# Optimization experiments

Hardware: AMD Instinct MI355X
Metric: run time of the kernel (lower is better)

## Reference

```python
import jax, jax.numpy as jnp
import numpy as np

EMB_DIM = 1024
N_HEADS = 16
HEAD_DIM = EMB_DIM // N_HEADS
WINDOW = 128
B, T = 4, 2048


def setup_inputs() -> dict:
    key = jax.random.key(0)
    k1, k2, k3 = jax.random.split(key, 3)
    x = jax.random.normal(k1, (B, T, EMB_DIM), dtype=jnp.float32)
    # nn.Linear weights: stored as [out, in], applied as x @ W^T
    s1 = 1.0 / np.sqrt(EMB_DIM)
    w_qkv = jax.random.uniform(k2, (3 * EMB_DIM, EMB_DIM), jnp.float32, -s1, s1)
    w_out = jax.random.uniform(k3, (EMB_DIM, EMB_DIM), jnp.float32, -s1, s1)
    return {"x": x, "w_qkv": w_qkv, "w_out": w_out}


def reference(x, w_qkv, w_out):
    Bs, Ts, C = x.shape
    scale = HEAD_DIM ** -0.5
    qkv = x @ w_qkv.T                                   # [B,T,3C]
    qkv = qkv.reshape(Bs, Ts, 3, N_HEADS, HEAD_DIM)
    qkv = jnp.transpose(qkv, (2, 0, 3, 1, 4))           # [3,B,H,T,D]
    q, k, v = qkv[0], qkv[1], qkv[2]
    scores = jnp.einsum('bhtd,bhsd->bhts', q, k) * scale  # [B,H,T,T]
    i = jnp.arange(Ts)[:, None]
    j = jnp.arange(Ts)[None, :]
    # causal AND within sliding window: i - WINDOW <= j <= i
    allowed = (j <= i) & (j >= i - WINDOW)               # [T,T] bool
    scores = jnp.where(allowed[None, None], scores, -jnp.inf)
    attn = jax.nn.softmax(scores, axis=-1)
    out = jnp.einsum('bhts,bhsd->bhtd', attn, v)         # [B,H,T,D]
    out = jnp.transpose(out, (0, 2, 1, 3)).reshape(Bs, Ts, C)
    return out @ w_out.T
```

## Files before the change

### kernel.cpp

```cpp
#include <hip/hip_runtime.h>
#include <hip/hip_bf16.h>
#include <stdint.h>

typedef __attribute__((ext_vector_type(8))) short bf16x8;
typedef __attribute__((ext_vector_type(4))) float f32x4;
typedef __attribute__((ext_vector_type(4))) unsigned short u16x4;

#define B_ 4
#define T_ 2048
#define C_ 1024
#define H_ 16
#define D_ 64

__device__ __forceinline__ unsigned short f2bf(float f) {
  union { float f; uint32_t u; } v; v.f = f;
  uint32_t u = v.u;
  uint32_t r = (u + 0x7FFFu + ((u >> 16) & 1u)) >> 16;
  return (unsigned short)r;
}

__device__ __forceinline__ void gload_lds16(const unsigned short* g, short* l) {
  __builtin_amdgcn_global_load_lds((__attribute__((address_space(1))) void*)(uintptr_t)g,
                                   (__attribute__((address_space(3))) void*)l, 16, 0, 0);
}

__global__ void __launch_bounds__(256) cast_f32_bf16(const float* __restrict__ src,
                                                     unsigned short* __restrict__ dst,
                                                     int n4) {
  int i = blockIdx.x * 256 + threadIdx.x;
  if (i >= n4) return;
  float4 f = ((const float4*)src)[i];
  u16x4 o;
  o[0] = f2bf(f.x); o[1] = f2bf(f.y); o[2] = f2bf(f.z); o[3] = f2bf(f.w);
  ((u16x4*)dst)[i] = o;
}

template <int MODE>
__global__ void __launch_bounds__(256) gemm_bt(const unsigned short* __restrict__ A,
                                               const unsigned short* __restrict__ Bm,
                                               unsigned short* __restrict__ qb,
                                               unsigned short* __restrict__ kb,
                                               unsigned short* __restrict__ vb,
                                               float* __restrict__ fo) {
  __shared__ short As[128 * 32];
  __shared__ short Bs[128 * 32];
  const int tid = threadIdx.x;
  const int bm = blockIdx.y * 128;
  const int bn = blockIdx.x * 128;
  const int w = tid >> 6;
  const int l = tid & 63;
  const int wm = w >> 1, wn = w & 1;
  const int lm = l & 15, lq = l >> 4;

  const int srow = w * 16 + (l >> 2);
  const int scol = (l & 3) * 8;
  const unsigned short* gA0 = A + (size_t)(bm + srow) * 1024 + scol;
  const unsigned short* gA1 = gA0 + (size_t)64 * 1024;
  const unsigned short* gB0 = Bm + (size_t)(bn + srow) * 1024 + scol;
  const unsigned short* gB1 = gB0 + (size_t)64 * 1024;
  short* dA0 = As + w * 512;
  short* dA1 = As + 2048 + w * 512;
  short* dB0 = Bs + w * 512;
  short* dB1 = Bs + 2048 + w * 512;

  f32x4 acc[4][4];
#pragma unroll
  for (int i = 0; i < 4; i++)
#pragma unroll
    for (int j = 0; j < 4; j++) acc[i][j] = (f32x4){0.f, 0.f, 0.f, 0.f};

  for (int k0 = 0; k0 < 1024; k0 += 32) {
    __syncthreads();
    gload_lds16(gA0 + k0, dA0);
    gload_lds16(gA1 + k0, dA1);
    gload_lds16(gB0 + k0, dB0);
    gload_lds16(gB1 + k0, dB1);
    __syncthreads();
    bf16x8 af[4], bfr[4];
#pragma unroll
    for (int i = 0; i < 4; i++)
      af[i] = *(const bf16x8*)&As[(wm * 64 + 16 * i + lm) * 32 + 8 * lq];
#pragma unroll
    for (int j = 0; j < 4; j++)
      bfr[j] = *(const bf16x8*)&Bs[(wn * 64 + 16 * j + lm) * 32 + 8 * lq];
#pragma unroll
    for (int i = 0; i < 4; i++)
#pragma unroll
      for (int j = 0; j < 4; j++)
        acc[i][j] = __builtin_amdgcn_mfma_f32_16x16x32_bf16(af[i], bfr[j], acc[i][j], 0, 0, 0);
  }

#pragma unroll
  for (int i = 0; i < 4; i++) {
#pragma unroll
    for (int j = 0; j < 4; j++) {
#pragma unroll
      for (int r = 0; r < 4; r++) {
        int m = bm + wm * 64 + 16 * i + 4 * lq + r;
        int n = bn + wn * 64 + 16 * j + lm;
        float val = acc[i][j][r];
        if (MODE == 0) {
          int which = n >> 10, rem = n & 1023;
          int h = rem >> 6, d = rem & 63;
          int b = m >> 11, t = m & 2047;
          unsigned short* dst = (which == 0) ? qb : ((which == 1) ? kb : vb);
          dst[(((size_t)(b * 16 + h)) * 2048 + t) * 64 + d] = f2bf(val);
        } else {
          fo[(size_t)m * 1024 + n] = val;
        }
      }
    }
  }
}

__global__ void __launch_bounds__(256) transpose_v(const unsigned short* __restrict__ Vb,
                                                   unsigned short* __restrict__ Vt) {
  __shared__ unsigned short Ls[64 * 66];
  const int tid = threadIdx.x;
  const int bh = blockIdx.y;
  const int t0 = blockIdx.x * 64;
  const size_t base = (size_t)bh * (T_ * D_);
  const int d0 = (tid & 7) * 8;
  const int it = tid >> 3;
#pragma unroll
  for (int p = 0; p < 2; p++) {
    int t = it + 32 * p;
    bf16x8 v = *(const bf16x8*)(Vb + base + (size_t)(t0 + t) * 64 + d0);
#pragma unroll
    for (int e = 0; e < 8; e++) Ls[(d0 + e) * 66 + t] = (unsigned short)v[e];
  }
  __syncthreads();
  const int d = tid >> 2;
  const int c = tid & 3;
  uint32_t r[8];
  const uint32_t* Lw = (const uint32_t*)&Ls[d * 66 + c * 16];
#pragma unroll
  for (int wj = 0; wj < 8; wj++) r[wj] = Lw[wj];
  unsigned short* o = Vt + base + (size_t)d * T_ + t0 + c * 16;
  *(uint4*)o = *(const uint4*)&r[0];
  *(uint4*)(o + 8) = *(const uint4*)&r[4];
}

__global__ void __launch_bounds__(256) attn_swa(const unsigned short* __restrict__ Qb,
                                               const unsigned short* __restrict__ Kb,
                                               const unsigned short* __restrict__ Vt,
                                               unsigned short* __restrict__ Ob) {
  __shared__ short P[4][16 * 40];
  const int wv = threadIdx.x >> 6;
  const int l = threadIdx.x & 63;
  const int wid = blockIdx.x * 4 + wv;
  const int bh = wid >> 7;
  const int t0 = (wid & 127) << 4;
  const int lm = l & 15, lq = l >> 4;
  const size_t base = (size_t)bh * (T_ * D_);

  bf16x8 aq0 = *(const bf16x8*)(Qb + base + (size_t)(t0 + lm) * 64 + 8 * lq);
  bf16x8 aq1 = *(const bf16x8*)(Qb + base + (size_t)(t0 + lm) * 64 + 32 + 8 * lq);

  float mst[4], lst[4];
  f32x4 Oa[4];
#pragma unroll
  for (int r = 0; r < 4; r++) { mst[r] = -1e30f; lst[r] = 0.f; }
#pragma unroll
  for (int jt = 0; jt < 4; jt++) Oa[jt] = (f32x4){0.f, 0.f, 0.f, 0.f};

  const float cs = 0.125f * 1.44269504f;
  int jstart = t0 - 128; if (jstart < 0) jstart = 0;

  for (int j0 = jstart; j0 < t0 + 16; j0 += 32) {
    f32x4 S[2];
#pragma unroll
    for (int hh = 0; hh < 2; hh++) {
      int kr = j0 + 16 * hh + lm; if (kr > T_ - 1) kr = T_ - 1;
      bf16x8 bk0 = *(const bf16x8*)(Kb + base + (size_t)kr * 64 + 8 * lq);
      bf16x8 bk1 = *(const bf16x8*)(Kb + base + (size_t)kr * 64 + 32 + 8 * lq);
      f32x4 s = (f32x4){0.f, 0.f, 0.f, 0.f};
      s = __builtin_amdgcn_mfma_f32_16x16x32_bf16(aq0, bk0, s, 0, 0, 0);
      s = __builtin_amdgcn_mfma_f32_16x16x32_bf16(aq1, bk1, s, 0, 0, 0);
      S[hh] = s;
    }
    float p0s[4], p1s[4], al[4];
#pragma unroll
    for (int r = 0; r < 4; r++) {
      int t = t0 + 4 * lq + r;
      int ja = j0 + lm, jb = j0 + 16 + lm;
      float s0 = ((ja <= t) && (ja + 128 >= t)) ? S[0][r] * cs : -1e30f;
      float s1 = ((jb <= t) && (jb + 128 >= t)) ? S[1][r] * cs : -1e30f;
      float m2 = fmaxf(s0, s1);
#pragma unroll
      for (int off = 1; off < 16; off <<= 1) m2 = fmaxf(m2, __shfl_xor(m2, off));
      float mn = fmaxf(mst[r], m2);
      float a = __builtin_amdgcn_exp2f(mst[r] - mn);
      float p0 = __builtin_amdgcn_exp2f(s0 - mn);
      float p1 = __builtin_amdgcn_exp2f(s1 - mn);
      float ps = p0 + p1;
#pragma unroll
      for (int off = 1; off < 16; off <<= 1) ps += __shfl_xor(ps, off);
      lst[r] = lst[r] * a + ps;
      mst[r] = mn;
      al[r] = a; p0s[r] = p0; p1s[r] = p1;
    }
#pragma unroll
    for (int jt = 0; jt < 4; jt++)
#pragma unroll
      for (int r = 0; r < 4; r++) Oa[jt][r] *= al[r];
#pragma unroll
    for (int r = 0; r < 4; r++) {
      P[wv][(4 * lq + r) * 40 + lm] = (short)f2bf(p0s[r]);
      P[wv][(4 * lq + r) * 40 + 16 + lm] = (short)f2bf(p1s[r]);
    }
    bf16x8 pa = *(const bf16x8*)&P[wv][lm * 40 + 8 * lq];
    int tb = j0 + 8 * lq;
    if (tb > T_ - 8) tb = T_ - 8;
#pragma unroll
    for (int jt = 0; jt < 4; jt++) {
      bf16x8 vf = *(const bf16x8*)(Vt + base + (size_t)(16 * jt + lm) * T_ + tb);
      Oa[jt] = __builtin_amdgcn_mfma_f32_16x16x32_bf16(pa, vf, Oa[jt], 0, 0, 0);
    }
  }
  const int b = bh >> 4, h = bh & 15;
#pragma unroll
  for (int r = 0; r < 4; r++) {
    float inv = 1.0f / lst[r];
    int t = t0 + 4 * lq + r;
#pragma unroll
    for (int jt = 0; jt < 4; jt++) {
      int c = h * 64 + 16 * jt + lm;
      Ob[((size_t)(b * T_ + t)) * 1024 + c] = f2bf(Oa[jt][r] * inv);
    }
  }
}

extern "C" void kernel_launch(void* const* d_in, const int* in_sizes, int n_in,
                              void* d_out, int out_size, void* d_ws, size_t ws_size,
                              hipStream_t stream) {
  const float* x = (const float*)d_in[0];
  const float* w_qkv = (const float*)d_in[1];
  const float* w_out = (const float*)d_in[2];
  float* out = (float*)d_out;

  unsigned short* xb = (unsigned short*)d_ws;
  unsigned short* wqkvb = xb + (size_t)8192 * 1024;
  unsigned short* woutb = wqkvb + (size_t)3072 * 1024;
  unsigned short* qb = woutb + (size_t)1024 * 1024;
  unsigned short* kb = qb + (size_t)64 * 2048 * 64;
  unsigned short* vb = kb + (size_t)64 * 2048 * 64;
  unsigned short* vtb = xb;
  unsigned short* ob = vb;

  cast_f32_bf16<<<8192, 256, 0, stream>>>(x, xb, 8192 * 1024 / 4);
  cast_f32_bf16<<<3072, 256, 0, stream>>>(w_qkv, wqkvb, 3072 * 1024 / 4);
  cast_f32_bf16<<<1024, 256, 0, stream>>>(w_out, woutb, 1024 * 1024 / 4);

  gemm_bt<0><<<dim3(24, 64), 256, 0, stream>>>(xb, wqkvb, qb, kb, vb, nullptr);
  transpose_v<<<dim3(32, 64), 256, 0, stream>>>(vb, vtb);
  attn_swa<<<2048, 256, 0, stream>>>(qb, kb, vtb, ob);
  gemm_bt<1><<<dim3(8, 64), 256, 0, stream>>>(ob, woutb, nullptr, nullptr, nullptr, out);
}
```

Measured before the change: 240.0 us.

## Replace online softmax with single-pass full-window softmax, fold scale into Q, merge casts

The attention kernel now computes all five 32-key score chunks covering the window up front and does one max and sum reduction, instead of an online softmax loop that rescaled the accumulators every chunk. The softmax scale and log2e factor are folded into Q when it is written out by the QKV GEMM epilogue. The three cast launches are merged into one. This costs more registers and LDS for the held scores and P tiles, and it always processes five chunks even for early rows where fewer are needed.

```diff
diff --git a/kernel.cpp b/kernel.cpp
--- a/kernel.cpp
+++ b/kernel.cpp
@@ -24,15 +24,21 @@
                                    (__attribute__((address_space(3))) void*)l, 16, 0, 0);
 }
 
-__global__ void __launch_bounds__(256) cast_f32_bf16(const float* __restrict__ src,
-                                                     unsigned short* __restrict__ dst,
-                                                     int n4) {
+__global__ void __launch_bounds__(256) cast3_f32_bf16(const float* __restrict__ x,
+                                                      const float* __restrict__ wq,
+                                                      const float* __restrict__ wo,
+                                                      unsigned short* __restrict__ xb,
+                                                      unsigned short* __restrict__ wqb,
+                                                      unsigned short* __restrict__ wob) {
   int i = blockIdx.x * 256 + threadIdx.x;
-  if (i >= n4) return;
-  float4 f = ((const float4*)src)[i];
+  const float* s; unsigned short* d; int off;
+  if (i < 2097152) { s = x; d = xb; off = i; }
+  else if (i < 2097152 + 786432) { s = wq; d = wqb; off = i - 2097152; }
+  else { s = wo; d = wob; off = i - 2883584; }
+  float4 f = ((const float4*)s)[off];
   u16x4 o;
   o[0] = f2bf(f.x); o[1] = f2bf(f.y); o[2] = f2bf(f.z); o[3] = f2bf(f.w);
-  ((u16x4*)dst)[i] = o;
+  ((u16x4*)d)[off] = o;
 }
 
 template <int MODE>
@@ -103,6 +109,7 @@
           int which = n >> 10, rem = n & 1023;
           int h = rem >> 6, d = rem & 63;
           int b = m >> 11, t = m & 2047;
+          if (which == 0) val *= 0.1803368801f;
           unsigned short* dst = (which == 0) ? qb : ((which == 1) ? kb : vb);
           dst[(((size_t)(b * 16 + h)) * 2048 + t) * 64 + d] = f2bf(val);
         } else {
@@ -145,7 +152,7 @@
                                                const unsigned short* __restrict__ Kb,
                                                const unsigned short* __restrict__ Vt,
                                                unsigned short* __restrict__ Ob) {
-  __shared__ short P[4][16 * 40];
+  __shared__ short P[4][5][16 * 40];
   const int wv = threadIdx.x >> 6;
   const int l = threadIdx.x & 63;
   const int wid = blockIdx.x * 4 + wv;
@@ -157,76 +164,88 @@
   bf16x8 aq0 = *(const bf16x8*)(Qb + base + (size_t)(t0 + lm) * 64 + 8 * lq);
   bf16x8 aq1 = *(const bf16x8*)(Qb + base + (size_t)(t0 + lm) * 64 + 32 + 8 * lq);
 
-  float mst[4], lst[4];
+  const int j0b = t0 - 144;
+  float sv[5][8];
+
+#pragma unroll
+  for (int c = 0; c < 5; c++) {
+    int j0 = j0b + 32 * c;
+#pragma unroll
+    for (int hh = 0; hh < 2; hh++) {
+      int kr = j0 + 16 * hh + lm; if (kr < 0) kr = 0;
+      const unsigned short* kp = Kb + base + (size_t)kr * 64;
+      bf16x8 b0 = *(const bf16x8*)(kp + 8 * lq);
+      bf16x8 b1 = *(const bf16x8*)(kp + 32 + 8 * lq);
+      f32x4 s = (f32x4){0.f, 0.f, 0.f, 0.f};
+      s = __builtin_amdgcn_mfma_f32_16x16x32_bf16(aq0, b0, s, 0, 0, 0);
+      s = __builtin_amdgcn_mfma_f32_16x16x32_bf16(aq1, b1, s, 0, 0, 0);
+#pragma unroll
+      for (int r = 0; r < 4; r++) sv[c][hh * 4 + r] = s[r];
+    }
+  }
+
+  float lsum[4];
+#pragma unroll
+  for (int r = 0; r < 4; r++) {
+    int t = t0 + 4 * lq + r;
+    int lo = t - 128; if (lo < 0) lo = 0;
+    float m2 = -1e30f;
+#pragma unroll
+    for (int c = 0; c < 5; c++)
+#pragma unroll
+      for (int hh = 0; hh < 2; hh++) {
+        int j = j0b + 32 * c + 16 * hh + lm;
+        float s = (j >= lo && j <= t) ? sv[c][hh * 4 + r] : -1e30f;
+        sv[c][hh * 4 + r] = s;
+        m2 = fmaxf(m2, s);
+      }
+#pragma unroll
+    for (int off = 1; off < 16; off <<= 1) m2 = fmaxf(m2, __shfl_xor(m2, off));
+    float ls = 0.f;
+#pragma unroll
+    for (int c = 0; c < 5; c++)
+#pragma unroll
+      for (int hh = 0; hh < 2; hh++) {
+        float p = __builtin_amdgcn_exp2f(sv[c][hh * 4 + r] - m2);
+        sv[c][hh * 4 + r] = p;
+        ls += p;
+      }
+#pragma unroll
+    for (int off = 1; off < 16; off <<= 1) ls += __shfl_xor(ls, off);
+    lsum[r] = ls;
+  }
+
+#pragma unroll
+  for (int c = 0; c < 5; c++)
+#pragma unroll
+    for (int r = 0; r < 4; r++)
+#pragma unroll
+      for (int hh = 0; hh < 2; hh++)
+        P[wv][c][(4 * lq + r) * 40 + 16 * hh + lm] = (short)f2bf(sv[c][hh * 4 + r]);
+
   f32x4 Oa[4];
 #pragma unroll
-  for (int r = 0; r < 4; r++) { mst[r] = -1e30f; lst[r] = 0.f; }
-#pragma unroll
   for (int jt = 0; jt < 4; jt++) Oa[jt] = (f32x4){0.f, 0.f, 0.f, 0.f};
-
-  const float cs = 0.125f * 1.44269504f;
-  int jstart = t0 - 128; if (jstart < 0) jstart = 0;
-
-  for (int j0 = jstart; j0 < t0 + 16; j0 += 32) {
-    f32x4 S[2];
-#pragma unroll
-    for (int hh = 0; hh < 2; hh++) {
-      int kr = j0 + 16 * hh + lm; if (kr > T_ - 1) kr = T_ - 1;
-      bf16x8 bk0 = *(const bf16x8*)(Kb + base + (size_t)kr * 64 + 8 * lq);
-      bf16x8 bk1 = *(const bf16x8*)(Kb + base + (size_t)kr * 64 + 32 + 8 * lq);
-      f32x4 s = (f32x4){0.f, 0.f, 0.f, 0.f};
-      s = __builtin_amdgcn_mfma_f32_16x16x32_bf16(aq0, bk0, s, 0, 0, 0);
-      s = __builtin_amdgcn_mfma_f32_16x16x32_bf16(aq1, bk1, s, 0, 0, 0);
-      S[hh] = s;
-    }
-    float p0s[4], p1s[4], al[4];
-#pragma unroll
-    for (int r = 0; r < 4; r++) {
-      int t = t0 + 4 * lq + r;
-      int ja = j0 + lm, jb = j0 + 16 + lm;
-      float s0 = ((ja <= t) && (ja + 128 >= t)) ? S[0][r] * cs : -1e30f;
-      float s1 = ((jb <= t) && (jb + 128 >= t)) ? S[1][r] * cs : -1e30f;
-      float m2 = fmaxf(s0, s1);
-#pragma unroll
-      for (int off = 1; off < 16; off <<= 1) m2 = fmaxf(m2, __shfl_xor(m2, off));
-      float mn = fmaxf(mst[r], m2);
-      float a = __builtin_amdgcn_exp2f(mst[r] - mn);
-      float p0 = __builtin_amdgcn_exp2f(s0 - mn);
-      float p1 = __builtin_amdgcn_exp2f(s1 - mn);
-      float ps = p0 + p1;
-#pragma unroll
-      for (int off = 1; off < 16; off <<= 1) ps += __shfl_xor(ps, off);
-      lst[r] = lst[r] * a + ps;
-      mst[r] = mn;
-      al[r] = a; p0s[r] = p0; p1s[r] = p1;
-    }
-#pragma unroll
-    for (int jt = 0; jt < 4; jt++)
-#pragma unroll
-      for (int r = 0; r < 4; r++) Oa[jt][r] *= al[r];
-#pragma unroll
-    for (int r = 0; r < 4; r++) {
-      P[wv][(4 * lq + r) * 40 + lm] = (short)f2bf(p0s[r]);
-      P[wv][(4 * lq + r) * 40 + 16 + lm] = (short)f2bf(p1s[r]);
-    }
-    bf16x8 pa = *(const bf16x8*)&P[wv][lm * 40 + 8 * lq];
-    int tb = j0 + 8 * lq;
-    if (tb > T_ - 8) tb = T_ - 8;
+#pragma unroll
+  for (int c = 0; c < 5; c++) {
+    bf16x8 pa = *(const bf16x8*)&P[wv][c][lm * 40 + 8 * lq];
+    int tb = j0b + 32 * c + 8 * lq; if (tb < 0) tb = 0;
 #pragma unroll
     for (int jt = 0; jt < 4; jt++) {
       bf16x8 vf = *(const bf16x8*)(Vt + base + (size_t)(16 * jt + lm) * T_ + tb);
       Oa[jt] = __builtin_amdgcn_mfma_f32_16x16x32_bf16(pa, vf, Oa[jt], 0, 0, 0);
     }
   }
+
   const int b = bh >> 4, h = bh & 15;
 #pragma unroll
   for (int r = 0; r < 4; r++) {
-    float inv = 1.0f / lst[r];
+    float inv = 1.0f / lsum[r];
     int t = t0 + 4 * lq + r;
 #pragma unroll
     for (int jt = 0; jt < 4; jt++) {
-      int c = h * 64 + 16 * jt + lm;
-      Ob[((size_t)(b * T_ + t)) * 1024 + c] = f2bf(Oa[jt][r] * inv);
+      int cc = h * 64 + 16 * jt + lm;
+      Ob[((size_t)(b * T_ + t)) * 1024 + cc] = f2bf(Oa[jt][r] * inv);
     }
   }
 }
@@ -248,10 +267,7 @@
   unsigned short* vtb = xb;
   unsigned short* ob = vb;
 
-  cast_f32_bf16<<<8192, 256, 0, stream>>>(x, xb, 8192 * 1024 / 4);
-  cast_f32_bf16<<<3072, 256, 0, stream>>>(w_qkv, wqkvb, 3072 * 1024 / 4);
-  cast_f32_bf16<<<1024, 256, 0, stream>>>(w_out, woutb, 1024 * 1024 / 4);
-
+  cast3_f32_bf16<<<12288, 256, 0, stream>>>(x, w_qkv, w_out, xb, wqkvb, woutb);
   gemm_bt<0><<<dim3(24, 64), 256, 0, stream>>>(xb, wqkvb, qb, kb, vb, nullptr);
   transpose_v<<<dim3(32, 64), 256, 0, stream>>>(vb, vtb);
   attn_swa<<<2048, 256, 0, stream>>>(qb, kb, vtb, ob);
```

New measurement: 240.0 us. No clear change (-0.0%).
